# Performance work log

Measured on AMD Instinct MI355X. Metric: run time of the kernel, lower is better.

Reference implementation:

```python
import jax, jax.numpy as jnp
import numpy as np

N_EMBD = 1024
HEAD_SIZE = 128
B, T = 8, 4096


def setup_inputs() -> dict:
    key = jax.random.key(0)
    ks = jax.random.split(key, 7)
    s = 1.0 / np.sqrt(N_EMBD)
    return {
        "x": jax.random.normal(ks[0], (B, T, N_EMBD), dtype=jnp.float32),
        "Wq": jax.random.uniform(ks[1], (N_EMBD, HEAD_SIZE), jnp.float32, -s, s),
        "bq": jax.random.uniform(ks[2], (HEAD_SIZE,), jnp.float32, -s, s),
        "Wk": jax.random.uniform(ks[3], (N_EMBD, HEAD_SIZE), jnp.float32, -s, s),
        "bk": jax.random.uniform(ks[4], (HEAD_SIZE,), jnp.float32, -s, s),
        "Wv": jax.random.uniform(ks[5], (N_EMBD, HEAD_SIZE), jnp.float32, -s, s),
        "bv": jax.random.uniform(ks[6], (HEAD_SIZE,), jnp.float32, -s, s),
    }


def reference(x, Wq, bq, Wk, bk, Wv, bv):
    # q,k,v: [B,T,H]
    q = x @ Wq + bq
    k = x @ Wk + bk
    v = x @ Wv + bv
    scale = HEAD_SIZE ** -0.5
    att = jnp.einsum("bth,bsh->bts", q, k) * scale  # [B,T,T]
    t = x.shape[1]
    causal = jnp.tril(jnp.ones((t, t), dtype=bool))
    att = jnp.where(causal, att, -jnp.inf)
    att = jax.nn.softmax(att, axis=-1)
    # dropout with p=0.0 is identity (eval-mode equivalent)
    out = jnp.einsum("bts,bsh->bth", att, v)  # [B,T,H]
    return out
```

## Files before the change

### kernel.cpp

```cpp
#include <hip/hip_runtime.h>
#include <hip/hip_bf16.h>
#include <stdint.h>

#define BATCH 8
#define SEQ   4096
#define EMB   1024
#define HD    128
#define NROWS 32768

typedef __attribute__((ext_vector_type(8))) short short8;
typedef __attribute__((ext_vector_type(4))) float f32x4;

__device__ inline unsigned short f2bf(float f) {
    union { float f; unsigned int u; } c; c.f = f;
    unsigned int u = c.u;
    unsigned int r = (u + 0x7fffu + ((u >> 16) & 1u)) >> 16;
    return (unsigned short)r;
}
__device__ inline float bf2f(unsigned short u) {
    union { unsigned int i; float f; } c; c.i = ((unsigned int)u) << 16; return c.f;
}
__device__ inline unsigned int pkbf(float a, float b) {
    __hip_bfloat162 h = __float22bfloat162_rn(make_float2(a, b));
    union { __hip_bfloat162 h; unsigned int u; } c; c.h = h; return c.u;
}

#define GLDS16(gp, lp) __builtin_amdgcn_global_load_lds( \
    (const __attribute__((address_space(1))) void*)(gp), \
    (__attribute__((address_space(3))) void*)(lp), 16, 0, 0)

__global__ __launch_bounds__(256) void prep_kernel(
    const float* __restrict__ Wq, const float* __restrict__ bq,
    const float* __restrict__ Wk, const float* __restrict__ bk,
    const float* __restrict__ Wv, const float* __restrict__ bv,
    unsigned short* __restrict__ wt, float* __restrict__ biasc)
{
    const int n = blockIdx.x;
    const int sel = n >> 7, h = n & 127;
    const float* W = (sel == 0) ? Wq : (sel == 1) ? Wk : Wv;
    const int tid = threadIdx.x;
    const int k0 = tid * 4;
    union { unsigned short us[4]; uint2 v; } pk;
#pragma unroll
    for (int u = 0; u < 4; ++u) pk.us[u] = f2bf(W[(size_t)(k0 + u) * HD + h]);
    *(uint2*)&wt[(size_t)n * EMB + k0] = pk.v;
    if (tid == 0) {
        const float* bp = (sel == 0) ? bq : (sel == 1) ? bk : bv;
        biasc[n] = bp[h];
    }
}

__global__ __launch_bounds__(512, 4) void gemm_qkv(
    const float* __restrict__ x, const unsigned short* __restrict__ wt,
    const float* __restrict__ biasc,
    unsigned short* __restrict__ q, unsigned short* __restrict__ kOut,
    unsigned short* __restrict__ vt)
{
    const int m0  = blockIdx.x * 64;
    const int tid = threadIdx.x;
    const int wave = tid >> 6, lane = tid & 63;
    const int quad = lane >> 4, l15 = lane & 15;

    __shared__ __align__(16) unsigned short As[2][64][40];
    __shared__ __align__(16) unsigned short Bs[2][12288];

    f32x4 acc[3][4];
#pragma unroll
    for (int i = 0; i < 3; ++i)
#pragma unroll
        for (int j = 0; j < 4; ++j) acc[i][j] = (f32x4){0.f, 0.f, 0.f, 0.f};

    const int arow = tid >> 3, akc = (tid & 7) * 4;
    float4 aR;

#define LOAD_A(kt) aR = *(const float4*)(x + (size_t)(m0 + arow) * EMB + (kt) * 32 + akc);
#define WRITE_A(buf)                                                        \
    {                                                                       \
        union { unsigned short us[4]; uint2 v; } pw;                        \
        pw.us[0] = f2bf(aR.x); pw.us[1] = f2bf(aR.y);                       \
        pw.us[2] = f2bf(aR.z); pw.us[3] = f2bf(aR.w);                       \
        *(uint2*)&As[buf][arow][akc] = pw.v;                                \
    }
#define STAGE_B(kt, buf)                                                    \
    {                                                                       \
        _Pragma("unroll")                                                   \
        for (int g = 0; g < 3; ++g) {                                       \
            int s0 = (g * 8 + wave) * 64;                                   \
            int s  = s0 + lane;                                             \
            int n  = s >> 2, c = (s & 3) ^ (n & 3);                         \
            GLDS16(wt + (size_t)n * EMB + (kt) * 32 + c * 8,                \
                   &Bs[buf][s0 * 8]);                                       \
        }                                                                   \
    }

    LOAD_A(0); STAGE_B(0, 0); WRITE_A(0);
    int cur = 0;

    for (int kt = 0; kt < 32; ++kt) {
        __syncthreads();
        if (kt < 31) { LOAD_A(kt + 1); STAGE_B(kt + 1, cur ^ 1); }
        short8 af[4], bw[3];
#pragma unroll
        for (int mj = 0; mj < 4; ++mj)
            af[mj] = *(const short8*)&As[cur][mj * 16 + l15][quad * 8];
#pragma unroll
        for (int ni = 0; ni < 3; ++ni) {
            int n = wave * 48 + ni * 16 + l15;
            bw[ni] = *(const short8*)&Bs[cur][n * 32 + ((quad ^ (n & 3)) << 3)];
        }
#pragma unroll
        for (int ni = 0; ni < 3; ++ni)
#pragma unroll
            for (int mj = 0; mj < 4; ++mj)
                acc[ni][mj] = __builtin_amdgcn_mfma_f32_16x16x32_bf16(
                    bw[ni], af[mj], acc[ni][mj], 0, 0, 0);
        if (kt < 31) WRITE_A(cur ^ 1);
        cur ^= 1;
    }

    const float qscale = 0.08838834764831845f * 1.4426950408889634f;
    const int bb = m0 >> 12;
    const int t0 = m0 & 4095;
#pragma unroll
    for (int ni = 0; ni < 3; ++ni) {
        int colbase = wave * 48 + ni * 16;
        int sel = colbase >> 7;
        int c0 = colbase + quad * 4;
        float4 bv4 = *(const float4*)&biasc[c0];
#pragma unroll
        for (int mj = 0; mj < 4; ++mj) {
            int m = m0 + mj * 16 + l15;
            if (sel == 0) {
                union { unsigned short us[4]; uint2 v; } pk;
#pragma unroll
                for (int j = 0; j < 4; ++j)
                    pk.us[j] = f2bf((acc[ni][mj][j] + ((const float*)&bv4)[j]) * qscale);
                *(uint2*)&q[(size_t)m * HD + (c0 & 127)] = pk.v;
            } else if (sel == 1) {
                union { unsigned short us[4]; uint2 v; } pk;
#pragma unroll
                for (int j = 0; j < 4; ++j)
                    pk.us[j] = f2bf(acc[ni][mj][j] + ((const float*)&bv4)[j]);
                *(uint2*)&kOut[(size_t)m * HD + (c0 & 127)] = pk.v;
            } else {
#pragma unroll
                for (int j = 0; j < 4; ++j) {
                    int h = (c0 & 127) + j;
                    vt[((size_t)(bb * 128 + h)) * SEQ + t0 + mj * 16 + l15] =
                        f2bf(acc[ni][mj][j] + ((const float*)&bv4)[j]);
                }
            }
        }
    }
#undef LOAD_A
#undef WRITE_A
#undef STAGE_B
}

__global__ __launch_bounds__(512, 2) void attn_kernel(
    const unsigned short* __restrict__ q, const unsigned short* __restrict__ k,
    const unsigned short* __restrict__ vt, float* __restrict__ outA,
    unsigned short* __restrict__ Oh, float2* __restrict__ ml)
{
    const int rank   = blockIdx.x;
    const int qtA    = 31 - (rank >> 4);
    const int parity = (rank >> 3) & 1;
    const int b      = rank & 7;
    const int tid  = threadIdx.x;
    const int wave = tid >> 6, lane = tid & 63;
    const int quad = lane >> 4, l15 = lane & 15;
    const int qtW   = (wave < 4) ? qtA : (31 - qtA);
    const int qrow0 = qtW * 128 + (wave & 3) * 32;
    const size_t qbase = (size_t)b * SEQ;
    const size_t vbase = (size_t)b * HD * SEQ;

    __shared__ __align__(16) unsigned short Ks[2][8192];
    __shared__ __align__(16) unsigned short Vs[2][8192];

#define STAGE_KV(kt_, buf_)                                                  \
    {                                                                        \
        _Pragma("unroll")                                                    \
        for (int g = 0; g < 2; ++g) {                                        \
            int s0 = (g * 8 + wave) * 64;                                    \
            int s  = s0 + lane;                                              \
            int key = s >> 4, c = (s & 15) ^ (key & 15);                     \
            GLDS16(k + (qbase + (kt_) * 64 + key) * HD + c * 8,              \
                   &Ks[buf_][s0 * 8]);                                       \
        }                                                                    \
        _Pragma("unroll")                                                    \
        for (int g = 0; g < 2; ++g) {                                        \
            int s0 = (g * 8 + wave) * 64;                                    \
            int s  = s0 + lane;                                              \
            int h = s >> 3, c = (s & 7) ^ (h & 7);                           \
            GLDS16(vt + vbase + (size_t)h * SEQ + (kt_) * 64 + c * 8,        \
                   &Vs[buf_][s0 * 8]);                                       \
        }                                                                    \
    }

    short8 qf[2][4];
#pragma unroll
    for (int mi = 0; mi < 2; ++mi)
#pragma unroll
        for (int kh = 0; kh < 4; ++kh)
            qf[mi][kh] = *(const short8*)(q + (qbase + qrow0 + mi * 16 + l15) * HD + kh * 32 + quad * 8);

    f32x4 o[2][8];
#pragma unroll
    for (int mi = 0; mi < 2; ++mi)
#pragma unroll
        for (int hi = 0; hi < 8; ++hi) o[mi][hi] = (f32x4){0.f, 0.f, 0.f, 0.f};
    float m_r[2] = {-1e30f, -1e30f};
    float l_r[2] = {0.f, 0.f};

    const int bpa0 = (l15 + 16 * ((2 * quad) & 3)) * 4;
    const int bpa1 = (l15 + 16 * ((2 * quad + 1) & 3)) * 4;

    const int niter = qtA + 1;
    STAGE_KV(parity, 0);
    int cur = 0;

    for (int i = 0; i < niter; ++i) {
        const int kt = parity + 2 * i;
        const int key0 = kt * 64;
        __syncthreads();
        if (i + 1 < niter) STAGE_KV(kt + 2, cur ^ 1);

        if (i <= qtW) {
            f32x4 s[2][4];
#pragma unroll
            for (int mi = 0; mi < 2; ++mi)
#pragma unroll
                for (int ni = 0; ni < 4; ++ni) s[mi][ni] = (f32x4){0.f, 0.f, 0.f, 0.f};
#pragma unroll
            for (int kh = 0; kh < 4; ++kh) {
#pragma unroll
                for (int ni = 0; ni < 4; ++ni) {
                    short8 kf = *(const short8*)&Ks[cur][(ni * 16 + l15) * 128 + (((kh * 4 + quad) ^ l15) << 3)];
                    s[0][ni] = __builtin_amdgcn_mfma_f32_16x16x32_bf16(kf, qf[0][kh], s[0][ni], 0, 0, 0);
                    s[1][ni] = __builtin_amdgcn_mfma_f32_16x16x32_bf16(kf, qf[1][kh], s[1][ni], 0, 0, 0);
                }
            }
            if (key0 + 63 > qrow0) {
#pragma unroll
                for (int mi = 0; mi < 2; ++mi)
#pragma unroll
                    for (int ni = 0; ni < 4; ++ni)
#pragma unroll
                        for (int j = 0; j < 4; ++j) {
                            int key = key0 + ni * 16 + quad * 4 + j;
                            int t   = qrow0 + mi * 16 + l15;
                            if (key > t) s[mi][ni][j] = -1e30f;
                        }
            }
            unsigned int pk[2][4][2];
#pragma unroll
            for (int mi = 0; mi < 2; ++mi) {
                float mx = -1e30f;
#pragma unroll
                for (int ni = 0; ni < 4; ++ni)
#pragma unroll
                    for (int j = 0; j < 4; ++j) mx = fmaxf(mx, s[mi][ni][j]);
                mx = fmaxf(mx, __shfl_xor(mx, 16));
                mx = fmaxf(mx, __shfl_xor(mx, 32));
                float mnew = fmaxf(m_r[mi], mx);
                float alpha = __builtin_amdgcn_exp2f(m_r[mi] - mnew);
                m_r[mi] = mnew;
                float rs = 0.f;
#pragma unroll
                for (int ni = 0; ni < 4; ++ni) {
                    float p0 = __builtin_amdgcn_exp2f(s[mi][ni][0] - mnew);
                    float p1 = __builtin_amdgcn_exp2f(s[mi][ni][1] - mnew);
                    float p2 = __builtin_amdgcn_exp2f(s[mi][ni][2] - mnew);
                    float p3 = __builtin_amdgcn_exp2f(s[mi][ni][3] - mnew);
                    rs += (p0 + p1) + (p2 + p3);
                    pk[mi][ni][0] = pkbf(p0, p1);
                    pk[mi][ni][1] = pkbf(p2, p3);
                }
                rs += __shfl_xor(rs, 16);
                rs += __shfl_xor(rs, 32);
                l_r[mi] = alpha * l_r[mi] + rs;
#pragma unroll
                for (int hi = 0; hi < 8; ++hi) o[mi][hi] *= alpha;
            }
            short8 pT[2][2];
#pragma unroll
            for (int mi = 0; mi < 2; ++mi)
#pragma unroll
                for (int sk = 0; sk < 2; ++sk) {
                    union { unsigned int u[4]; short8 s8; } pt;
                    int lo = 2 * sk, hi_ = 2 * sk + 1;
                    unsigned int a0 = (unsigned)__builtin_amdgcn_ds_bpermute(bpa0, (int)pk[mi][lo][0]);
                    unsigned int b0 = (unsigned)__builtin_amdgcn_ds_bpermute(bpa0, (int)pk[mi][hi_][0]);
                    pt.u[0] = (quad < 2) ? a0 : b0;
                    unsigned int a1 = (unsigned)__builtin_amdgcn_ds_bpermute(bpa0, (int)pk[mi][lo][1]);
                    unsigned int b1 = (unsigned)__builtin_amdgcn_ds_bpermute(bpa0, (int)pk[mi][hi_][1]);
                    pt.u[1] = (quad < 2) ? a1 : b1;
                    unsigned int a2 = (unsigned)__builtin_amdgcn_ds_bpermute(bpa1, (int)pk[mi][lo][0]);
                    unsigned int b2 = (unsigned)__builtin_amdgcn_ds_bpermute(bpa1, (int)pk[mi][hi_][0]);
                    pt.u[2] = (quad < 2) ? a2 : b2;
                    unsigned int a3 = (unsigned)__builtin_amdgcn_ds_bpermute(bpa1, (int)pk[mi][lo][1]);
                    unsigned int b3 = (unsigned)__builtin_amdgcn_ds_bpermute(bpa1, (int)pk[mi][hi_][1]);
                    pt.u[3] = (quad < 2) ? a3 : b3;
                    pT[mi][sk] = pt.s8;
                }
#pragma unroll
            for (int sk = 0; sk < 2; ++sk)
#pragma unroll
                for (int hi = 0; hi < 8; ++hi) {
                    short8 vf = *(const short8*)&Vs[cur][(hi * 16 + l15) * 64 + (((sk * 4 + quad) ^ (l15 & 7)) << 3)];
                    o[0][hi] = __builtin_amdgcn_mfma_f32_16x16x32_bf16(vf, pT[0][sk], o[0][hi], 0, 0, 0);
                    o[1][hi] = __builtin_amdgcn_mfma_f32_16x16x32_bf16(vf, pT[1][sk], o[1][hi], 0, 0, 0);
                }
        }
        cur ^= 1;
    }

#pragma unroll
    for (int mi = 0; mi < 2; ++mi) {
        size_t rowg = qbase + qrow0 + mi * 16 + l15;
        if (quad == 0) ml[(size_t)parity * NROWS + rowg] = make_float2(m_r[mi], l_r[mi]);
#pragma unroll
        for (int hi = 0; hi < 8; ++hi) {
            if (parity == 0) {
                *(f32x4*)&outA[rowg * HD + hi * 16 + quad * 4] = o[mi][hi];
            } else {
                union { unsigned short us[4]; uint2 v; } pw;
#pragma unroll
                for (int j = 0; j < 4; ++j) pw.us[j] = f2bf(o[mi][hi][j]);
                *(uint2*)&Oh[rowg * HD + hi * 16 + quad * 4] = pw.v;
            }
        }
    }
#undef STAGE_KV
}

__global__ __launch_bounds__(256) void merge_kernel(
    float* __restrict__ out, const unsigned short* __restrict__ Oh,
    const float2* __restrict__ ml)
{
    int idx = blockIdx.x * 256 + threadIdx.x;
    int row = idx >> 5;
    int hc  = (idx & 31) << 2;
    float2 a = ml[row];
    float2 c = ml[NROWS + row];
    float M  = fmaxf(a.x, c.x);
    float w0 = __builtin_amdgcn_exp2f(a.x - M);
    float w1 = __builtin_amdgcn_exp2f(c.x - M);
    float inv = 1.0f / (w0 * a.y + w1 * c.y);
    f32x4 o0 = *(const f32x4*)&out[(size_t)row * HD + hc];
    union { unsigned short us[4]; uint2 v; } pv;
    pv.v = *(const uint2*)&Oh[(size_t)row * HD + hc];
    f32x4 r;
#pragma unroll
    for (int j = 0; j < 4; ++j)
        r[j] = (w0 * o0[j] + w1 * bf2f(pv.us[j])) * inv;
    *(f32x4*)&out[(size_t)row * HD + hc] = r;
}

extern "C" void kernel_launch(void* const* d_in, const int* in_sizes, int n_in,
                              void* d_out, int out_size, void* d_ws, size_t ws_size,
                              hipStream_t stream) {
    const float* x  = (const float*)d_in[0];
    const float* Wq = (const float*)d_in[1];
    const float* bq = (const float*)d_in[2];
    const float* Wk = (const float*)d_in[3];
    const float* bk = (const float*)d_in[4];
    const float* Wv = (const float*)d_in[5];
    const float* bv = (const float*)d_in[6];
    float* out = (float*)d_out;

    unsigned short* wt    = (unsigned short*)d_ws;
    float*          biasc = (float*)((char*)d_ws + 786432);
    unsigned short* qb    = (unsigned short*)((char*)d_ws + 787968);
    unsigned short* kb    = qb  + (size_t)NROWS * HD;
    unsigned short* vtb   = kb  + (size_t)NROWS * HD;
    unsigned short* Oh    = vtb + (size_t)NROWS * HD;
    float2*         ml    = (float2*)((char*)d_ws + 787968 + 4ull * NROWS * HD * 2);

    prep_kernel<<<dim3(384), 256, 0, stream>>>(Wq, bq, Wk, bk, Wv, bv, wt, biasc);
    gemm_qkv<<<dim3(512), 512, 0, stream>>>(x, wt, biasc, qb, kb, vtb);
    attn_kernel<<<dim3(256), 512, 0, stream>>>(qb, kb, vtb, out, Oh, ml);
    merge_kernel<<<dim3(NROWS * 32 / 256), 256, 0, stream>>>(out, Oh, ml);
}
```

Baseline: 319.9 us.

## Load attention K/V straight from global and triple-buffer the QKV GEMM A tile

The attention kernel drops its LDS double-buffered K/V staging and its block-wide barriers. Each wave now reads K and V^T fragments directly from global memory and exits early once its causal range is done. Launch becomes 512 blocks of 256 threads, one query tile each, instead of 256 blocks that each paired two tiles. The QKV GEMM moves to a triple-buffered, XOR-swizzled A tile in LDS, loads A two steps ahead through two register slots, and changes the B swizzle to cut bank conflicts and stalls around the barrier. Each wave now fetches K/V itself instead of sharing one staged copy, so the attention path relies on cache hits, and global load latency is no longer hidden behind an async prefetch.

```diff
diff --git a/kernel.cpp b/kernel.cpp
--- a/kernel.cpp
+++ b/kernel.cpp
@@ -61,7 +61,7 @@
     const int wave = tid >> 6, lane = tid & 63;
     const int quad = lane >> 4, l15 = lane & 15;
 
-    __shared__ __align__(16) unsigned short As[2][64][40];
+    __shared__ __align__(16) unsigned short As[3][2048];
     __shared__ __align__(16) unsigned short Bs[2][12288];
 
     f32x4 acc[3][4];
@@ -71,15 +71,16 @@
         for (int j = 0; j < 4; ++j) acc[i][j] = (f32x4){0.f, 0.f, 0.f, 0.f};
 
     const int arow = tid >> 3, akc = (tid & 7) * 4;
-    float4 aR;
-
-#define LOAD_A(kt) aR = *(const float4*)(x + (size_t)(m0 + arow) * EMB + (kt) * 32 + akc);
-#define WRITE_A(buf)                                                        \
+    const int awidx = arow * 32 + ((((akc >> 3) ^ ((arow >> 1) & 3))) << 3) + (akc & 7);
+    float4 aR[2];
+
+#define LOAD_A(kt, slot) aR[slot] = *(const float4*)(x + (size_t)(m0 + arow) * EMB + (kt) * 32 + akc);
+#define WRITE_A(buf, slot)                                                  \
     {                                                                       \
         union { unsigned short us[4]; uint2 v; } pw;                        \
-        pw.us[0] = f2bf(aR.x); pw.us[1] = f2bf(aR.y);                       \
-        pw.us[2] = f2bf(aR.z); pw.us[3] = f2bf(aR.w);                       \
-        *(uint2*)&As[buf][arow][akc] = pw.v;                                \
+        pw.us[0] = f2bf(aR[slot].x); pw.us[1] = f2bf(aR[slot].y);           \
+        pw.us[2] = f2bf(aR[slot].z); pw.us[3] = f2bf(aR[slot].w);           \
+        *(uint2*)&As[buf][awidx] = pw.v;                                    \
     }
 #define STAGE_B(kt, buf)                                                    \
     {                                                                       \
@@ -87,26 +88,32 @@
         for (int g = 0; g < 3; ++g) {                                       \
             int s0 = (g * 8 + wave) * 64;                                   \
             int s  = s0 + lane;                                             \
-            int n  = s >> 2, c = (s & 3) ^ (n & 3);                         \
+            int n  = s >> 2, csw = s & 3;                                   \
+            int c  = csw ^ ((n >> 1) & 3);                                  \
             GLDS16(wt + (size_t)n * EMB + (kt) * 32 + c * 8,                \
                    &Bs[buf][s0 * 8]);                                       \
         }                                                                   \
     }
 
-    LOAD_A(0); STAGE_B(0, 0); WRITE_A(0);
-    int cur = 0;
-
+    LOAD_A(0, 0); LOAD_A(1, 1);
+    STAGE_B(0, 0); STAGE_B(1, 1);
+    WRITE_A(0, 0);
+    LOAD_A(2, 0);
+
+    int cur3 = 0;
     for (int kt = 0; kt < 32; ++kt) {
         __syncthreads();
-        if (kt < 31) { LOAD_A(kt + 1); STAGE_B(kt + 1, cur ^ 1); }
+        if (kt >= 1 && kt < 31) STAGE_B(kt + 1, (kt + 1) & 1);
         short8 af[4], bw[3];
 #pragma unroll
-        for (int mj = 0; mj < 4; ++mj)
-            af[mj] = *(const short8*)&As[cur][mj * 16 + l15][quad * 8];
+        for (int mj = 0; mj < 4; ++mj) {
+            int row = mj * 16 + l15;
+            af[mj] = *(const short8*)&As[cur3][row * 32 + ((quad ^ ((row >> 1) & 3)) << 3)];
+        }
 #pragma unroll
         for (int ni = 0; ni < 3; ++ni) {
             int n = wave * 48 + ni * 16 + l15;
-            bw[ni] = *(const short8*)&Bs[cur][n * 32 + ((quad ^ (n & 3)) << 3)];
+            bw[ni] = *(const short8*)&Bs[kt & 1][n * 32 + ((quad ^ ((n >> 1) & 3)) << 3)];
         }
 #pragma unroll
         for (int ni = 0; ni < 3; ++ni)
@@ -114,8 +121,12 @@
             for (int mj = 0; mj < 4; ++mj)
                 acc[ni][mj] = __builtin_amdgcn_mfma_f32_16x16x32_bf16(
                     bw[ni], af[mj], acc[ni][mj], 0, 0, 0);
-        if (kt < 31) WRITE_A(cur ^ 1);
-        cur ^= 1;
+        if (kt < 31) {
+            int nxt3 = (cur3 == 2) ? 0 : cur3 + 1;
+            WRITE_A(nxt3, (kt + 1) & 1);
+            cur3 = nxt3;
+        }
+        if (kt < 30) LOAD_A(kt + 2, kt & 1);
     }
 
     const float qscale = 0.08838834764831845f * 1.4426950408889634f;
@@ -157,45 +168,21 @@
 #undef STAGE_B
 }
 
-__global__ __launch_bounds__(512, 2) void attn_kernel(
+__global__ __launch_bounds__(256, 2) void attn_kernel(
     const unsigned short* __restrict__ q, const unsigned short* __restrict__ k,
     const unsigned short* __restrict__ vt, float* __restrict__ outA,
     unsigned short* __restrict__ Oh, float2* __restrict__ ml)
 {
     const int rank   = blockIdx.x;
-    const int qtA    = 31 - (rank >> 4);
+    const int qt     = 31 - (rank >> 4);
     const int parity = (rank >> 3) & 1;
     const int b      = rank & 7;
     const int tid  = threadIdx.x;
     const int wave = tid >> 6, lane = tid & 63;
     const int quad = lane >> 4, l15 = lane & 15;
-    const int qtW   = (wave < 4) ? qtA : (31 - qtA);
-    const int qrow0 = qtW * 128 + (wave & 3) * 32;
+    const int qrow0 = qt * 128 + wave * 32;
     const size_t qbase = (size_t)b * SEQ;
     const size_t vbase = (size_t)b * HD * SEQ;
-
-    __shared__ __align__(16) unsigned short Ks[2][8192];
-    __shared__ __align__(16) unsigned short Vs[2][8192];
-
-#define STAGE_KV(kt_, buf_)                                                  \
-    {                                                                        \
-        _Pragma("unroll")                                                    \
-        for (int g = 0; g < 2; ++g) {                                        \
-            int s0 = (g * 8 + wave) * 64;                                    \
-            int s  = s0 + lane;                                              \
-            int key = s >> 4, c = (s & 15) ^ (key & 15);                     \
-            GLDS16(k + (qbase + (kt_) * 64 + key) * HD + c * 8,              \
-                   &Ks[buf_][s0 * 8]);                                       \
-        }                                                                    \
-        _Pragma("unroll")                                                    \
-        for (int g = 0; g < 2; ++g) {                                        \
-            int s0 = (g * 8 + wave) * 64;                                    \
-            int s  = s0 + lane;                                              \
-            int h = s >> 3, c = (s & 7) ^ (h & 7);                           \
-            GLDS16(vt + vbase + (size_t)h * SEQ + (kt_) * 64 + c * 8,        \
-                   &Vs[buf_][s0 * 8]);                                       \
-        }                                                                    \
-    }
 
     short8 qf[2][4];
 #pragma unroll
@@ -215,104 +202,107 @@
     const int bpa0 = (l15 + 16 * ((2 * quad) & 3)) * 4;
     const int bpa1 = (l15 + 16 * ((2 * quad + 1) & 3)) * 4;
 
-    const int niter = qtA + 1;
-    STAGE_KV(parity, 0);
-    int cur = 0;
-
+    const int niter = qt + 1;
     for (int i = 0; i < niter; ++i) {
         const int kt = parity + 2 * i;
         const int key0 = kt * 64;
-        __syncthreads();
-        if (i + 1 < niter) STAGE_KV(kt + 2, cur ^ 1);
-
-        if (i <= qtW) {
-            f32x4 s[2][4];
+        if (key0 > qrow0 + 31) break;
+
+        short8 kf[4][4];
+#pragma unroll
+        for (int kh = 0; kh < 4; ++kh)
+#pragma unroll
+            for (int ni = 0; ni < 4; ++ni)
+                kf[kh][ni] = *(const short8*)(k + (qbase + key0 + ni * 16 + l15) * HD + kh * 32 + quad * 8);
+
+        f32x4 s[2][4];
+#pragma unroll
+        for (int mi = 0; mi < 2; ++mi)
+#pragma unroll
+            for (int ni = 0; ni < 4; ++ni) s[mi][ni] = (f32x4){0.f, 0.f, 0.f, 0.f};
+#pragma unroll
+        for (int kh = 0; kh < 4; ++kh)
+#pragma unroll
+            for (int ni = 0; ni < 4; ++ni) {
+                s[0][ni] = __builtin_amdgcn_mfma_f32_16x16x32_bf16(kf[kh][ni], qf[0][kh], s[0][ni], 0, 0, 0);
+                s[1][ni] = __builtin_amdgcn_mfma_f32_16x16x32_bf16(kf[kh][ni], qf[1][kh], s[1][ni], 0, 0, 0);
+            }
+        if (key0 + 63 > qrow0) {
 #pragma unroll
             for (int mi = 0; mi < 2; ++mi)
 #pragma unroll
-                for (int ni = 0; ni < 4; ++ni) s[mi][ni] = (f32x4){0.f, 0.f, 0.f, 0.f};
-#pragma unroll
-            for (int kh = 0; kh < 4; ++kh) {
-#pragma unroll
-                for (int ni = 0; ni < 4; ++ni) {
-                    short8 kf = *(const short8*)&Ks[cur][(ni * 16 + l15) * 128 + (((kh * 4 + quad) ^ l15) << 3)];
-                    s[0][ni] = __builtin_amdgcn_mfma_f32_16x16x32_bf16(kf, qf[0][kh], s[0][ni], 0, 0, 0);
-                    s[1][ni] = __builtin_amdgcn_mfma_f32_16x16x32_bf16(kf, qf[1][kh], s[1][ni], 0, 0, 0);
-                }
-            }
-            if (key0 + 63 > qrow0) {
-#pragma unroll
-                for (int mi = 0; mi < 2; ++mi)
-#pragma unroll
-                    for (int ni = 0; ni < 4; ++ni)
-#pragma unroll
-                        for (int j = 0; j < 4; ++j) {
-                            int key = key0 + ni * 16 + quad * 4 + j;
-                            int t   = qrow0 + mi * 16 + l15;
-                            if (key > t) s[mi][ni][j] = -1e30f;
-                        }
-            }
-            unsigned int pk[2][4][2];
-#pragma unroll
-            for (int mi = 0; mi < 2; ++mi) {
-                float mx = -1e30f;
-#pragma unroll
                 for (int ni = 0; ni < 4; ++ni)
 #pragma unroll
-                    for (int j = 0; j < 4; ++j) mx = fmaxf(mx, s[mi][ni][j]);
-                mx = fmaxf(mx, __shfl_xor(mx, 16));
-                mx = fmaxf(mx, __shfl_xor(mx, 32));
-                float mnew = fmaxf(m_r[mi], mx);
-                float alpha = __builtin_amdgcn_exp2f(m_r[mi] - mnew);
-                m_r[mi] = mnew;
-                float rs = 0.f;
-#pragma unroll
-                for (int ni = 0; ni < 4; ++ni) {
-                    float p0 = __builtin_amdgcn_exp2f(s[mi][ni][0] - mnew);
-                    float p1 = __builtin_amdgcn_exp2f(s[mi][ni][1] - mnew);
-                    float p2 = __builtin_amdgcn_exp2f(s[mi][ni][2] - mnew);
-                    float p3 = __builtin_amdgcn_exp2f(s[mi][ni][3] - mnew);
-                    rs += (p0 + p1) + (p2 + p3);
-                    pk[mi][ni][0] = pkbf(p0, p1);
-                    pk[mi][ni][1] = pkbf(p2, p3);
-                }
-                rs += __shfl_xor(rs, 16);
-                rs += __shfl_xor(rs, 32);
-                l_r[mi] = alpha * l_r[mi] + rs;
-#pragma unroll
-                for (int hi = 0; hi < 8; ++hi) o[mi][hi] *= alpha;
-            }
-            short8 pT[2][2];
-#pragma unroll
-            for (int mi = 0; mi < 2; ++mi)
-#pragma unroll
-                for (int sk = 0; sk < 2; ++sk) {
-                    union { unsigned int u[4]; short8 s8; } pt;
-                    int lo = 2 * sk, hi_ = 2 * sk + 1;
-                    unsigned int a0 = (unsigned)__builtin_amdgcn_ds_bpermute(bpa0, (int)pk[mi][lo][0]);
-                    unsigned int b0 = (unsigned)__builtin_amdgcn_ds_bpermute(bpa0, (int)pk[mi][hi_][0]);
-                    pt.u[0] = (quad < 2) ? a0 : b0;
-                    unsigned int a1 = (unsigned)__builtin_amdgcn_ds_bpermute(bpa0, (int)pk[mi][lo][1]);
-                    unsigned int b1 = (unsigned)__builtin_amdgcn_ds_bpermute(bpa0, (int)pk[mi][hi_][1]);
-                    pt.u[1] = (quad < 2) ? a1 : b1;
-                    unsigned int a2 = (unsigned)__builtin_amdgcn_ds_bpermute(bpa1, (int)pk[mi][lo][0]);
-                    unsigned int b2 = (unsigned)__builtin_amdgcn_ds_bpermute(bpa1, (int)pk[mi][hi_][0]);
-                    pt.u[2] = (quad < 2) ? a2 : b2;
-                    unsigned int a3 = (unsigned)__builtin_amdgcn_ds_bpermute(bpa1, (int)pk[mi][lo][1]);
-                    unsigned int b3 = (unsigned)__builtin_amdgcn_ds_bpermute(bpa1, (int)pk[mi][hi_][1]);
-                    pt.u[3] = (quad < 2) ? a3 : b3;
-                    pT[mi][sk] = pt.s8;
-                }
-#pragma unroll
-            for (int sk = 0; sk < 2; ++sk)
-#pragma unroll
-                for (int hi = 0; hi < 8; ++hi) {
-                    short8 vf = *(const short8*)&Vs[cur][(hi * 16 + l15) * 64 + (((sk * 4 + quad) ^ (l15 & 7)) << 3)];
-                    o[0][hi] = __builtin_amdgcn_mfma_f32_16x16x32_bf16(vf, pT[0][sk], o[0][hi], 0, 0, 0);
-                    o[1][hi] = __builtin_amdgcn_mfma_f32_16x16x32_bf16(vf, pT[1][sk], o[1][hi], 0, 0, 0);
-                }
-        }
-        cur ^= 1;
+                    for (int j = 0; j < 4; ++j) {
+                        int key = key0 + ni * 16 + quad * 4 + j;
+                        int t   = qrow0 + mi * 16 + l15;
+                        if (key > t) s[mi][ni][j] = -1e30f;
+                    }
+        }
+        unsigned int pk[2][4][2];
+#pragma unroll
+        for (int mi = 0; mi < 2; ++mi) {
+            float mx = -1e30f;
+#pragma unroll
+            for (int ni = 0; ni < 4; ++ni)
+#pragma unroll
+                for (int j = 0; j < 4; ++j) mx = fmaxf(mx, s[mi][ni][j]);
+            mx = fmaxf(mx, __shfl_xor(mx, 16));
+            mx = fmaxf(mx, __shfl_xor(mx, 32));
+            float mnew = fmaxf(m_r[mi], mx);
+            float alpha = __builtin_amdgcn_exp2f(m_r[mi] - mnew);
+            m_r[mi] = mnew;
+            float rs = 0.f;
+#pragma unroll
+            for (int ni = 0; ni < 4; ++ni) {
+                float p0 = __builtin_amdgcn_exp2f(s[mi][ni][0] - mnew);
+                float p1 = __builtin_amdgcn_exp2f(s[mi][ni][1] - mnew);
+                float p2 = __builtin_amdgcn_exp2f(s[mi][ni][2] - mnew);
+                float p3 = __builtin_amdgcn_exp2f(s[mi][ni][3] - mnew);
+                rs += (p0 + p1) + (p2 + p3);
+                pk[mi][ni][0] = pkbf(p0, p1);
+                pk[mi][ni][1] = pkbf(p2, p3);
+            }
+            rs += __shfl_xor(rs, 16);
+            rs += __shfl_xor(rs, 32);
+            l_r[mi] = alpha * l_r[mi] + rs;
+#pragma unroll
+            for (int hi = 0; hi < 8; ++hi) o[mi][hi] *= alpha;
+        }
+        short8 pT[2][2];
+#pragma unroll
+        for (int mi = 0; mi < 2; ++mi)
+#pragma unroll
+            for (int sk = 0; sk < 2; ++sk) {
+                union { unsigned int u[4]; short8 s8; } pt;
+                int lo = 2 * sk, hi_ = 2 * sk + 1;
+                unsigned int a0 = (unsigned)__builtin_amdgcn_ds_bpermute(bpa0, (int)pk[mi][lo][0]);
+                unsigned int b0 = (unsigned)__builtin_amdgcn_ds_bpermute(bpa0, (int)pk[mi][hi_][0]);
+                pt.u[0] = (quad < 2) ? a0 : b0;
+                unsigned int a1 = (unsigned)__builtin_amdgcn_ds_bpermute(bpa0, (int)pk[mi][lo][1]);
+                unsigned int b1 = (unsigned)__builtin_amdgcn_ds_bpermute(bpa0, (int)pk[mi][hi_][1]);
+                pt.u[1] = (quad < 2) ? a1 : b1;
+                unsigned int a2 = (unsigned)__builtin_amdgcn_ds_bpermute(bpa1, (int)pk[mi][lo][0]);
+                unsigned int b2 = (unsigned)__builtin_amdgcn_ds_bpermute(bpa1, (int)pk[mi][hi_][0]);
+                pt.u[2] = (quad < 2) ? a2 : b2;
+                unsigned int a3 = (unsigned)__builtin_amdgcn_ds_bpermute(bpa1, (int)pk[mi][lo][1]);
+                unsigned int b3 = (unsigned)__builtin_amdgcn_ds_bpermute(bpa1, (int)pk[mi][hi_][1]);
+                pt.u[3] = (quad < 2) ? a3 : b3;
+                pT[mi][sk] = pt.s8;
+            }
+        short8 vf[2][8];
+#pragma unroll
+        for (int sk = 0; sk < 2; ++sk)
+#pragma unroll
+            for (int hi = 0; hi < 8; ++hi)
+                vf[sk][hi] = *(const short8*)(vt + vbase + (size_t)(hi * 16 + l15) * SEQ + key0 + sk * 32 + quad * 8);
+#pragma unroll
+        for (int sk = 0; sk < 2; ++sk)
+#pragma unroll
+            for (int hi = 0; hi < 8; ++hi) {
+                o[0][hi] = __builtin_amdgcn_mfma_f32_16x16x32_bf16(vf[sk][hi], pT[0][sk], o[0][hi], 0, 0, 0);
+                o[1][hi] = __builtin_amdgcn_mfma_f32_16x16x32_bf16(vf[sk][hi], pT[1][sk], o[1][hi], 0, 0, 0);
+            }
     }
 
 #pragma unroll
@@ -331,7 +321,6 @@
             }
         }
     }
-#undef STAGE_KV
 }
 
 __global__ __launch_bounds__(256) void merge_kernel(
@@ -379,6 +368,6 @@
 
     prep_kernel<<<dim3(384), 256, 0, stream>>>(Wq, bq, Wk, bk, Wv, bv, wt, biasc);
     gemm_qkv<<<dim3(512), 512, 0, stream>>>(x, wt, biasc, qb, kb, vtb);
-    attn_kernel<<<dim3(256), 512, 0, stream>>>(qb, kb, vtb, out, Oh, ml);
+    attn_kernel<<<dim3(512), 256, 0, stream>>>(qb, kb, vtb, out, Oh, ml);
     merge_kernel<<<dim3(NROWS * 32 / 256), 256, 0, stream>>>(out, Oh, ml);
 }
```

New measurement: 426.2 us. +33.2%, slower.
